# Kernel optimization log

Hardware: AMD Instinct MI355X
Metric: run time of the kernel (lower is better)

## Reference

```python
import jax, jax.numpy as jnp
import numpy as np

B, T, C, NH, L, V = 4, 1024, 768, 12, 4, 512
HD = C // NH
EPS = 1e-5


def setup_inputs() -> dict:
    key = jax.random.key(0)
    ks = jax.random.split(key, 16)
    std = 0.02
    n = lambda k, shape: jax.random.normal(k, shape, jnp.float32) * std
    return {
        "idx": jax.random.randint(ks[0], (B, T), 0, V),
        "tok_emb": n(ks[1], (V, C)),
        "type_emb": n(ks[2], (2, C)),
        "pos_emb": n(ks[3], (1, T, C)),
        "ln1_s": jnp.ones((L, C)), "ln1_b": jnp.zeros((L, C)),
        "ln2_s": jnp.ones((L, C)), "ln2_b": jnp.zeros((L, C)),
        "wq": n(ks[4], (L, C, C)), "bq": jnp.zeros((L, C)),
        "wk": n(ks[5], (L, C, C)), "bk": jnp.zeros((L, C)),
        "wv": n(ks[6], (L, C, C)), "bv": jnp.zeros((L, C)),
        "wp": n(ks[7], (L, C, C)), "bp": jnp.zeros((L, C)),
        "w1": n(ks[8], (L, C, 4 * C)), "b1": jnp.zeros((L, 4 * C)),
        "w2": n(ks[9], (L, 4 * C, C)), "b2": jnp.zeros((L, C)),
        "lnf_s": jnp.ones((C,)), "lnf_b": jnp.zeros((C,)),
        "head_w": n(ks[10], (C, V)),
    }


def _ln(x, s, b):
    m = jnp.mean(x, axis=-1, keepdims=True)
    v = jnp.mean((x - m) ** 2, axis=-1, keepdims=True)
    return (x - m) * jax.lax.rsqrt(v + EPS) * s + b


def _forward(idx, tok_emb, type_emb, pos_emb, ln1_s, ln1_b, ln2_s, ln2_b,
             wq, bq, wk, bk, wv, bv, wp, bp, w1, b1, w2, b2, lnf_s, lnf_b, head_w):
    t = idx.shape[1]
    # token + position + type(=1) embeddings; dropout is identity in eval mode
    x = tok_emb[idx] + pos_emb[:, :t, :] + type_emb[1]
    causal = jnp.tril(jnp.ones((t, t), dtype=bool))  # [T,T]
    scale = 1.0 / np.sqrt(HD)
    attn_maps = []
    for l in range(L):
        h = _ln(x, ln1_s[l], ln1_b[l])
        # project and split heads -> [B,NH,T,HD]
        def heads(w, bb):
            return (h @ w + bb).reshape(B, t, NH, HD).transpose(0, 2, 1, 3)
        q, k, v = heads(wq[l], bq[l]), heads(wk[l], bk[l]), heads(wv[l], bv[l])
        att = jnp.einsum('bhqd,bhkd->bhqk', q, k) * scale
        att = jnp.where(causal, att, -jnp.inf)
        att = jax.nn.softmax(att, axis=-1)
        attn_maps.append(att)
        y = jnp.einsum('bhqk,bhkd->bhqd', att, v)
        y = y.transpose(0, 2, 1, 3).reshape(B, t, C)
        x = x + (y @ wp[l] + bp[l])
        h2 = _ln(x, ln2_s[l], ln2_b[l])
        x = x + (jax.nn.gelu(h2 @ w1[l] + b1[l], approximate=False) @ w2[l] + b2[l])
    x = _ln(x, lnf_s, lnf_b)
    logits = x @ head_w  # head has no bias
    return logits, jnp.stack(attn_maps, axis=0)  # [L,B,NH,T,T]


def reference(idx, tok_emb, type_emb, pos_emb, ln1_s, ln1_b, ln2_s, ln2_b,
              wq, bq, wk, bk, wv, bv, wp, bp, w1, b1, w2, b2, lnf_s, lnf_b, head_w):
    return _forward(idx, tok_emb, type_emb, pos_emb, ln1_s, ln1_b, ln2_s, ln2_b,
                    wq, bq, wk, bk, wv, bv, wp, bp, w1, b1, w2, b2, lnf_s, lnf_b, head_w)
```

## Files before the change

### kernel.cpp

```cpp
#include <hip/hip_runtime.h>
#include <cstdint>


#define B_ 4
#define T_ 1024
#define C_ 768
#define NH_ 12
#define HD_ 64
#define L_ 4
#define V_ 512
#define C4_ 3072

typedef unsigned short u16;
typedef float f32x4 __attribute__((ext_vector_type(4)));
typedef short s16x8 __attribute__((ext_vector_type(8)));
typedef u16 u16x4 __attribute__((ext_vector_type(4)));
typedef u16 u16x8 __attribute__((ext_vector_type(8)));

__device__ __forceinline__ u16 f2b(float f){
  union { float f; unsigned u; } v; v.f = f;
  unsigned u = v.u + 0x7fffu + ((v.u >> 16) & 1u);
  return (u16)(u >> 16);
}

__device__ __forceinline__ unsigned cvtpk(float lo, float hi){
  unsigned r;
  asm("v_cvt_pk_bf16_f32 %0, %1, %2" : "=v"(r) : "v"(lo), "v"(hi));
  return r;
}

__device__ __forceinline__ f32x4 mfma16(s16x8 a, s16x8 b, f32x4 c){
  return __builtin_amdgcn_mfma_f32_16x16x32_bf16(a, b, c, 0, 0, 0);
}

__device__ __forceinline__ void gload16(const void* g, void* l){
  __builtin_amdgcn_global_load_lds((const __attribute__((address_space(1))) unsigned*)g,
                                   (__attribute__((address_space(3))) unsigned*)l, 16, 0, 0);
}

__global__ __launch_bounds__(256) void embed_ln_kernel(const int* __restrict__ idx,
    const float* __restrict__ tok, const float* __restrict__ pos, const float* __restrict__ typ,
    const float* __restrict__ g, const float* __restrict__ bta,
    float* __restrict__ x, u16* __restrict__ out){
  int lane = threadIdx.x & 63;
  int w = threadIdx.x >> 6;
  int row = blockIdx.x*4 + w;
  int t = row & (T_-1);
  int tk = idx[row];
  const float* tr = tok + (size_t)tk*C_;
  const float* pr = pos + (size_t)t*C_;
  float4 v[3];
  float s = 0.f;
  #pragma unroll
  for (int j=0;j<3;j++){
    int c = j*256 + lane*4;
    float4 a = *(const float4*)(tr + c);
    float4 p = *(const float4*)(pr + c);
    float4 ty = *(const float4*)(typ + c);
    v[j] = (float4){a.x+p.x+ty.x, a.y+p.y+ty.y, a.z+p.z+ty.z, a.w+p.w+ty.w};
    s += v[j].x + v[j].y + v[j].z + v[j].w;
  }
  #pragma unroll
  for (int o=32;o>0;o>>=1) s += __shfl_xor(s, o, 64);
  float mean = s * (1.0f/C_);
  float var = 0.f;
  #pragma unroll
  for (int j=0;j<3;j++){
    float dx=v[j].x-mean, dy=v[j].y-mean, dz=v[j].z-mean, dw=v[j].w-mean;
    var += dx*dx+dy*dy+dz*dz+dw*dw;
  }
  #pragma unroll
  for (int o=32;o>0;o>>=1) var += __shfl_xor(var, o, 64);
  float rs = rsqrtf(var*(1.0f/C_) + 1e-5f);
  float* xr = x + (size_t)row*C_;
  u16* orow = out + (size_t)row*C_;
  #pragma unroll
  for (int j=0;j<3;j++){
    int c = j*256 + lane*4;
    *(float4*)(xr + c) = v[j];
    float4 gg = *(const float4*)(g + c);
    float4 bb = *(const float4*)(bta + c);
    u16x4 o = { f2b((v[j].x-mean)*rs*gg.x + bb.x), f2b((v[j].y-mean)*rs*gg.y + bb.y),
                f2b((v[j].z-mean)*rs*gg.z + bb.z), f2b((v[j].w-mean)*rs*gg.w + bb.w) };
    *(u16x4*)(orow + c) = o;
  }
}

__global__ __launch_bounds__(256) void ln_kernel(const float* __restrict__ x,
    const float* __restrict__ g, const float* __restrict__ bta, u16* __restrict__ out){
  int lane = threadIdx.x & 63;
  int row = blockIdx.x*4 + (threadIdx.x >> 6);
  const float* xr = x + (size_t)row*C_;
  float v[12];
  float s = 0.f;
  #pragma unroll
  for (int j=0;j<12;j++){ v[j] = xr[lane + j*64]; s += v[j]; }
  #pragma unroll
  for (int o=32;o>0;o>>=1) s += __shfl_xor(s, o, 64);
  float mean = s * (1.0f/C_);
  float var = 0.f;
  #pragma unroll
  for (int j=0;j<12;j++){ float d = v[j]-mean; var += d*d; }
  #pragma unroll
  for (int o=32;o>0;o>>=1) var += __shfl_xor(var, o, 64);
  float rs = rsqrtf(var*(1.0f/C_) + 1e-5f);
  u16* orow = out + (size_t)row*C_;
  #pragma unroll
  for (int j=0;j<12;j++){ int c = lane+j*64; orow[c] = f2b((v[j]-mean)*rs*g[c] + bta[c]); }
}

struct ConvTable {
  const float* src[7];
  u16* dst[7];
  int K[7], N[7], nTN[7], perZ[7];
  unsigned long long outStride[7];
  int start[8];
};

__global__ __launch_bounds__(256) void convT_all(ConvTable tab){
  int bid = blockIdx.x;
  int d = 0;
  #pragma unroll
  for (int j=1;j<7;j++) if (bid >= tab.start[j]) d = j;
  const float* src = nullptr; u16* dst = nullptr;
  int K=0, N=0, nTN=0, perZ=0; size_t oS=0;
  #pragma unroll
  for (int j=0;j<7;j++) if (d==j){ src=tab.src[j]; dst=tab.dst[j]; K=tab.K[j]; N=tab.N[j];
                                   nTN=tab.nTN[j]; perZ=tab.perZ[j]; oS=(size_t)tab.outStride[j]; }
  int local = bid - tab.start[d];
  int z = local / perZ;
  int rem = local - z*perZ;
  int tk = rem / nTN;
  int tn = rem - tk*nTN;
  int k0 = tk*64, n0 = tn*64;
  size_t inBase = (size_t)z * K * N;
  size_t outBase = (size_t)z * oS;

  __shared__ u16 t[64][68];
  #pragma unroll
  for (int rep=0;rep<4;rep++){
    int id = threadIdx.x + rep*256;
    int kr = id >> 4;
    int nc = (id & 15)*4;
    float4 v = *(const float4*)(src + inBase + (size_t)(k0+kr)*N + n0+nc);
    t[nc+0][kr] = f2b(v.x);
    t[nc+1][kr] = f2b(v.y);
    t[nc+2][kr] = f2b(v.z);
    t[nc+3][kr] = f2b(v.w);
  }
  __syncthreads();
  #pragma unroll
  for (int rep=0;rep<4;rep++){
    int id = threadIdx.x + rep*256;
    int nr = id >> 4;
    int kc = (id & 15)*4;
    u16x4 o = {t[nr][kc], t[nr][kc+1], t[nr][kc+2], t[nr][kc+3]};
    *(u16x4*)(dst + outBase + (size_t)(n0+nr)*K + k0+kc) = o;
  }
}

template<int BM, int MODE, bool GELU>
__global__ __launch_bounds__(256) void gemm_kernel(
    const u16* __restrict__ A, const u16* __restrict__ Bt,
    const float* __restrict__ bias, const float* __restrict__ bias2, const float* __restrict__ bias3,
    u16* __restrict__ outb, u16* __restrict__ outk, u16* __restrict__ outv,
    float* __restrict__ outf, int N, int K)
{
  constexpr int MT = BM/32;
  constexpr int BUF = (BM+128)*64;
  __shared__ u16 smem[2*BUF];
  const int tid = threadIdx.x;
  const int lane = tid & 63;
  const int w = tid >> 6;
  const int wm = w >> 1, wn = w & 1;

  const int gx = gridDim.x;
  const int nwg = gx * gridDim.y;
  int flat = blockIdx.y*gx + blockIdx.x;
  int swzb = (flat & 7)*(nwg >> 3) + (flat >> 3);
  const int m0 = (swzb / gx) * BM;
  const int n0 = (swzb % gx) * 128;

  const int cl = lane & 15, gr = lane >> 4;
  const int rsub = lane >> 3;
  const int swl = ((lane & 7) ^ rsub) * 8;

  f32x4 acc[MT][4];
  #pragma unroll
  for (int a=0;a<MT;a++)
    #pragma unroll
    for (int b=0;b<4;b++) acc[a][b] = (f32x4){0.f,0.f,0.f,0.f};

  auto stage = [&](int kk, u16* buf){
    u16* la = buf;
    u16* lb = buf + BM*64;
    #pragma unroll
    for (int j=0;j<MT;j++){
      int rowb = w*(BM/4) + j*8;
      gload16(A + (size_t)(m0+rowb+rsub)*K + kk + swl, &la[rowb*64]);
    }
    #pragma unroll
    for (int j=0;j<4;j++){
      int rowb = w*32 + j*8;
      gload16(Bt + (size_t)(n0+rowb+rsub)*K + kk + swl, &lb[rowb*64]);
    }
  };

  const int nSteps = K >> 6;
  stage(0, smem);

  for (int t=0; t<nSteps; t++){
    u16* cur = smem + (t&1)*BUF;
    u16* nxt = smem + ((t+1)&1)*BUF;
    if (t+1 < nSteps){
      stage((t+1)<<6, nxt);
      if constexpr (BM==128) asm volatile("s_waitcnt vmcnt(8)" ::: "memory");
      else                   asm volatile("s_waitcnt vmcnt(6)" ::: "memory");
    } else {
      asm volatile("s_waitcnt vmcnt(0)" ::: "memory");
    }
    __builtin_amdgcn_sched_barrier(0);
    __builtin_amdgcn_s_barrier();

    u16* la = cur;
    u16* lb = cur + BM*64;
    #pragma unroll
    for (int cc=0;cc<2;cc++){
      int ko = cc*32 + gr*8;
      s16x8 af[MT], bf[4];
      #pragma unroll
      for (int mt=0;mt<MT;mt++){
        int row = wm*(BM/2) + mt*16 + cl;
        af[mt] = *(const s16x8*)&la[row*64 + (ko ^ ((row&7)*8))];
      }
      #pragma unroll
      for (int nt=0;nt<4;nt++){
        int row = wn*64 + nt*16 + cl;
        bf[nt] = *(const s16x8*)&lb[row*64 + (ko ^ ((row&7)*8))];
      }
      #pragma unroll
      for (int mt=0;mt<MT;mt++)
        #pragma unroll
        for (int nt=0;nt<4;nt++)
          acc[mt][nt] = mfma16(af[mt], bf[nt], acc[mt][nt]);
    }
    __builtin_amdgcn_sched_barrier(0);
    __builtin_amdgcn_s_barrier();
  }

  if (MODE == 5){
    const int which = n0 / C_;
    if (which < 2){
      u16* outp = which ? outk : outb;
      const float* bp = which ? bias2 : bias;
      const int nb = n0 - which*C_;
      #pragma unroll
      for (int mt=0;mt<MT;mt++){
        #pragma unroll
        for (int nt=0;nt<4;nt++){
          #pragma unroll
          for (int i=0;i<4;i++){
            int tl = wm*64 + mt*16 + gr*4 + i;
            int dl = wn*64 + nt*16 + cl;
            smem[tl*128 + (dl ^ ((tl&7)*8))] = f2b(acc[mt][nt][i] + bp[nb + dl]);
          }
        }
      }
      __syncthreads();
      int r = tid >> 1;
      int hloc = tid & 1;
      int h = (nb >> 6) + hloc;
      int b = m0 >> 10, tg = (m0 & (T_-1)) + r;
      u16* orow = outp + (((size_t)b*NH_ + h)*T_ + tg)*HD_;
      #pragma unroll
      for (int j=0;j<8;j++){
        int ch = hloc*8 + j;
        u16x8 vv = *(const u16x8*)&smem[r*128 + ((ch ^ (r&7))*8)];
        *(u16x8*)&orow[j*8] = vv;
      }
    } else {
      const int nb = n0 - 2*C_;
      #pragma unroll
      for (int mt=0;mt<MT;mt++){
        #pragma unroll
        for (int nt=0;nt<4;nt++){
          #pragma unroll
          for (int i=0;i<4;i++){
            int tl = wm*64 + mt*16 + gr*4 + i;
            int dl = wn*64 + nt*16 + cl;
            smem[tl*128 + (dl ^ ((tl&7)*8))] = f2b(acc[mt][nt][i] + bias3[nb + dl]);
          }
        }
      }
      __syncthreads();
      int r = tid & 127, half = tid >> 7;
      int dg = nb + r;
      int h = dg >> 6, dd = dg & (HD_-1);
      int b = m0 >> 10, tg = m0 & (T_-1);
      u16* orow = outv + (((size_t)b*NH_ + h)*HD_ + dd)*T_ + tg;
      #pragma unroll
      for (int j=0;j<8;j++){
        int t0 = half*64 + j*8;
        u16x8 vv;
        #pragma unroll
        for (int s2=0;s2<8;s2++){
          int t = t0 + s2;
          vv[s2] = smem[t*128 + (r ^ ((t&7)*8))];
        }
        *(u16x8*)&orow[t0] = vv;
      }
    }
  } else if (MODE == 0){
    #pragma unroll
    for (int mt=0;mt<MT;mt++){
      #pragma unroll
      for (int nt=0;nt<4;nt++){
        #pragma unroll
        for (int i=0;i<4;i++){
          int tl = wm*64 + mt*16 + gr*4 + i;
          int dl = wn*64 + nt*16 + cl;
          float val = acc[mt][nt][i] + bias[n0 + dl];
          if (GELU) val = 0.5f*val*(1.0f + erff(val*0.70710678118654752440f));
          smem[tl*128 + (dl ^ ((tl&7)*8))] = f2b(val);
        }
      }
    }
    __syncthreads();
    int r = tid >> 1;
    int halfc = tid & 1;
    u16* orow = outb + (size_t)(m0 + r)*N + n0 + halfc*64;
    #pragma unroll
    for (int j=0;j<8;j++){
      int ch = halfc*8 + j;
      u16x8 vv = *(const u16x8*)&smem[r*128 + ((ch ^ (r&7))*8)];
      *(u16x8*)&orow[j*8] = vv;
    }
  } else {
    #pragma unroll
    for (int mt=0;mt<MT;mt++){
      #pragma unroll
      for (int nt=0;nt<4;nt++){
        #pragma unroll
        for (int i=0;i<4;i++){
          int gm = m0 + wm*(BM/2) + mt*16 + gr*4 + i;
          int gn = n0 + wn*64 + nt*16 + cl;
          float val = acc[mt][nt][i];
          if (bias) val += bias[gn];
          if (MODE == 3){
            outf[(size_t)gm*N + gn] += val;
          } else {
            outf[(size_t)gm*N + gn] = val;
          }
        }
      }
    }
  }
}

__global__ __launch_bounds__(256,2) void attn_kernel(
    const u16* __restrict__ q, const u16* __restrict__ k, const u16* __restrict__ vt,
    float* __restrict__ att, u16* __restrict__ y, int layer)
{
  __shared__ u16 pl[4][16*64];
  const int lane = threadIdx.x & 63;
  const int w = threadIdx.x >> 6;
  const int qt = blockIdx.x;
  const int bh = blockIdx.y;
  const int bb = bh / NH_;
  const int hh = bh - bb*NH_;
  const int q0 = qt*64 + w*16;
  const u16* qbase = q + (size_t)bh*T_*HD_;
  const u16* kbase = k + (size_t)bh*T_*HD_;
  const u16* vbase = vt + (size_t)bh*HD_*T_;
  float* abase = att + ((size_t)layer*B_*NH_ + bh)*((size_t)T_*T_);
  u16* plw = &pl[w][0];

  const int cl = lane & 15, gr = lane >> 4;
  const int d0 = gr*8;
  const int swz = (cl & 7)*8;
  const int myq = q0 + cl;

  s16x8 qf0 = *(const s16x8*)(qbase + (size_t)(q0+cl)*HD_ + d0);
  s16x8 qf1 = *(const s16x8*)(qbase + (size_t)(q0+cl)*HD_ + 32 + d0);

  const float scale = 0.125f;
  const int nkt = qt + 1;

  unsigned pbuf[16][8];
  float slocal = 0.f;
  f32x4 yacc[4];
  #pragma unroll
  for (int n=0;n<4;n++) yacc[n] = (f32x4){0.f,0.f,0.f,0.f};

  #pragma unroll
  for (int kt=0; kt<16; kt++){
    if (kt < nkt){
      #pragma unroll
      for (int n=0;n<4;n++){
        int krow = kt*64 + n*16 + cl;
        s16x8 kf0 = *(const s16x8*)(kbase + (size_t)krow*HD_ + d0);
        s16x8 kf1 = *(const s16x8*)(kbase + (size_t)krow*HD_ + 32 + d0);
        f32x4 dacc = (f32x4){0.f,0.f,0.f,0.f};
        dacc = mfma16(kf0, qf0, dacc);
        dacc = mfma16(kf1, qf1, dacc);
        float p[4];
        #pragma unroll
        for (int i=0;i<4;i++){
          float sv = dacc[i]*scale;
          int kk = kt*64 + n*16 + gr*4 + i;
          if (kt == qt && kk > myq) sv = -1e30f;
          p[i] = __expf(sv);
        }
        slocal += (p[0]+p[1]) + (p[2]+p[3]);
        unsigned lo = cvtpk(p[0],p[1]), hi = cvtpk(p[2],p[3]);
        pbuf[kt][2*n]   = lo;
        pbuf[kt][2*n+1] = hi;
        int colb = (n*16 + gr*4) ^ swz;
        *(uint2*)&plw[cl*64 + colb] = make_uint2(lo, hi);
      }
      asm volatile("s_waitcnt lgkmcnt(0)" ::: "memory");
      __builtin_amdgcn_sched_barrier(0);
      #pragma unroll
      for (int cc=0;cc<2;cc++){
        s16x8 pa = *(const s16x8*)&plw[cl*64 + ((cc*32 + d0) ^ swz)];
        #pragma unroll
        for (int n2=0;n2<4;n2++){
          s16x8 bv = *(const s16x8*)(vbase + (size_t)(n2*16+cl)*T_ + kt*64 + cc*32 + d0);
          yacc[n2] = mfma16(pa, bv, yacc[n2]);
        }
      }
    }
  }

  slocal += __shfl_xor(slocal, 16, 64);
  slocal += __shfl_xor(slocal, 32, 64);
  float inv = 1.0f / slocal;

  float invy[4];
  #pragma unroll
  for (int i=0;i<4;i++) invy[i] = __shfl(inv, gr*4 + i, 64);

  #pragma unroll
  for (int n2=0;n2<4;n2++){
    #pragma unroll
    for (int i=0;i<4;i++){
      int r = q0 + gr*4 + i;
      y[((size_t)bb*T_ + r)*C_ + hh*HD_ + n2*16 + cl] = f2b(yacc[n2][i]*invy[i]);
    }
  }

  #pragma unroll
  for (int kt=0; kt<16; kt++){
    if (kt < nkt){
      #pragma unroll
      for (int n=0;n<4;n++){
        unsigned lo = pbuf[kt][2*n], hi = pbuf[kt][2*n+1];
        float p0 = __uint_as_float(lo << 16)          * inv;
        float p1 = __uint_as_float(lo & 0xffff0000u)  * inv;
        float p2 = __uint_as_float(hi << 16)          * inv;
        float p3 = __uint_as_float(hi & 0xffff0000u)  * inv;
        *(float4*)&abase[(size_t)myq*T_ + kt*64 + n*16 + gr*4] = make_float4(p0,p1,p2,p3);
      }
    }
  }

  int kend = nkt*64;
  if (kend < T_){
    int w4 = (T_ - kend) >> 2;
    for (int r = w; r < 64; r += 4){
      float* rp = abase + (size_t)(qt*64 + r)*T_ + kend;
      for (int c = lane; c < w4; c += 64){
        *(float4*)(rp + c*4) = make_float4(0.f,0.f,0.f,0.f);
      }
    }
  }
}

extern "C" void kernel_launch(void* const* d_in, const int* in_sizes, int n_in,
                              void* d_out, int out_size, void* d_ws, size_t ws_size,
                              hipStream_t stream)
{
  (void)in_sizes; (void)n_in; (void)out_size; (void)ws_size;
  const int*   idx  = (const int*)d_in[0];
  const float* tok  = (const float*)d_in[1];
  const float* typ  = (const float*)d_in[2];
  const float* pos  = (const float*)d_in[3];
  const float* ln1s = (const float*)d_in[4];
  const float* ln1b = (const float*)d_in[5];
  const float* ln2s = (const float*)d_in[6];
  const float* ln2b = (const float*)d_in[7];
  const float* wq   = (const float*)d_in[8];
  const float* bq   = (const float*)d_in[9];
  const float* wk   = (const float*)d_in[10];
  const float* bk   = (const float*)d_in[11];
  const float* wv   = (const float*)d_in[12];
  const float* bv   = (const float*)d_in[13];
  const float* wp   = (const float*)d_in[14];
  const float* bp   = (const float*)d_in[15];
  const float* w1   = (const float*)d_in[16];
  const float* b1   = (const float*)d_in[17];
  const float* w2   = (const float*)d_in[18];
  const float* b2   = (const float*)d_in[19];
  const float* lnfs = (const float*)d_in[20];
  const float* lnfb = (const float*)d_in[21];
  const float* hw   = (const float*)d_in[22];

  char* ws = (char*)d_ws;
  float* x    = (float*)(ws + 0);
  u16* hbf    = (u16*)(ws + 12582912);
  u16* qb     = (u16*)(ws + 18874368);
  u16* kb     = (u16*)(ws + 25165824);
  u16* vtb    = (u16*)(ws + 31457280);
  u16* yb     = (u16*)(ws + 37748736);
  u16* h2     = (u16*)(ws + 44040192);
  u16* wqkvT  = (u16*)(ws + 69206016);
  u16* wpT    = (u16*)(ws + 83361792);
  u16* w1T    = (u16*)(ws + 88080384);
  u16* w2T    = (u16*)(ws + 106954752);
  u16* hwT    = (u16*)(ws + 125829120);

  float* logits = (float*)d_out;
  float* att = logits + (size_t)B_*T_*V_;

  const size_t CC   = (size_t)C_*C_;
  const size_t CC4  = (size_t)C_*C4_;
  const size_t QKVL = (size_t)3*C_*C_;

  ConvTable tab;
  const float* srcs[7] = {wq, wk, wv, wp, w1, w2, hw};
  u16* dsts[7] = {wqkvT, wqkvT + CC, wqkvT + 2*CC, wpT, w1T, w2T, hwT};
  int Ks[7]   = {C_, C_, C_, C_, C_,  C4_, C_};
  int Ns[7]   = {C_, C_, C_, C_, C4_, C_,  V_};
  int nzs[7]  = {L_, L_, L_, L_, L_,  L_,  1};
  unsigned long long oss[7] = {QKVL, QKVL, QKVL, CC, CC4, CC4, CC};
  int acc = 0;
  for (int j=0;j<7;j++){
    tab.src[j]=srcs[j]; tab.dst[j]=dsts[j]; tab.K[j]=Ks[j]; tab.N[j]=Ns[j];
    tab.nTN[j]=Ns[j]/64; tab.perZ[j]=(Ks[j]/64)*(Ns[j]/64); tab.outStride[j]=oss[j];
    tab.start[j]=acc; acc += tab.perZ[j]*nzs[j];
  }
  tab.start[7]=acc;
  convT_all<<<acc, 256, 0, stream>>>(tab);

  embed_ln_kernel<<<1024, 256, 0, stream>>>(idx, tok, pos, typ + C_, ln1s, ln1b, x, hbf);

  for (int l=0; l<L_; l++){
    if (l > 0)
      ln_kernel<<<1024, 256, 0, stream>>>(x, ln1s + l*C_, ln1b + l*C_, hbf);
    gemm_kernel<128,5,false><<<dim3(18,32), 256, 0, stream>>>(
        hbf, wqkvT + l*QKVL, bq + l*C_, bk + l*C_, bv + l*C_,
        qb, kb, vtb, nullptr, 3*C_, C_);
    attn_kernel<<<dim3(16,48), 256, 0, stream>>>(qb, kb, vtb, att, yb, l);
    gemm_kernel<128,3,false><<<dim3(6,32), 256, 0, stream>>>(
        yb, wpT + l*CC, bp + l*C_, nullptr, nullptr,
        nullptr, nullptr, nullptr, x, C_, C_);
    ln_kernel<<<1024, 256, 0, stream>>>(x, ln2s + l*C_, ln2b + l*C_, hbf);
    gemm_kernel<128,0,true><<<dim3(24,32), 256, 0, stream>>>(
        hbf, w1T + l*CC4, b1 + l*C4_, nullptr, nullptr,
        h2, nullptr, nullptr, nullptr, C4_, C_);
    gemm_kernel<128,3,false><<<dim3(6,32), 256, 0, stream>>>(
        h2, w2T + l*CC4, b2 + l*C_, nullptr, nullptr,
        nullptr, nullptr, nullptr, x, C_, C4_);
  }
  ln_kernel<<<1024, 256, 0, stream>>>(x, lnfs, lnfb, hbf);
  gemm_kernel<64,4,false><<<dim3(4,64), 256, 0, stream>>>(
      hbf, hwT, nullptr, nullptr, nullptr,
      nullptr, nullptr, nullptr, logits, V_, C_);
}
```

Baseline: 1.237 ms.

## Single-buffer GEMM LDS staging and raise wave priority around attention MFMAs

The GEMM kernel's double-buffered LDS pipeline, which prefetched the next K tile during compute, is replaced by one buffer loaded and then consumed behind __syncthreads each step. This halves LDS use per block and may allow more resident blocks, but global loads no longer overlap with MFMA work. Separately, the attention kernel wraps its MFMA sequences in s_setprio(1)/s_setprio(0) so waves issuing matrix work get scheduling priority.

```diff
diff --git a/kernel.cpp b/kernel.cpp
--- a/kernel.cpp
+++ b/kernel.cpp
@@ -167,8 +167,7 @@
     float* __restrict__ outf, int N, int K)
 {
   constexpr int MT = BM/32;
-  constexpr int BUF = (BM+128)*64;
-  __shared__ u16 smem[2*BUF];
+  __shared__ u16 smem[(BM+128)*64];
   const int tid = threadIdx.x;
   const int lane = tid & 63;
   const int w = tid >> 6;
@@ -191,9 +190,12 @@
     #pragma unroll
     for (int b=0;b<4;b++) acc[a][b] = (f32x4){0.f,0.f,0.f,0.f};
 
-  auto stage = [&](int kk, u16* buf){
-    u16* la = buf;
-    u16* lb = buf + BM*64;
+  u16* la = smem;
+  u16* lb = smem + BM*64;
+
+  const int nSteps = K >> 6;
+  for (int t=0; t<nSteps; t++){
+    const int kk = t << 6;
     #pragma unroll
     for (int j=0;j<MT;j++){
       int rowb = w*(BM/4) + j*8;
@@ -204,26 +206,7 @@
       int rowb = w*32 + j*8;
       gload16(Bt + (size_t)(n0+rowb+rsub)*K + kk + swl, &lb[rowb*64]);
     }
-  };
-
-  const int nSteps = K >> 6;
-  stage(0, smem);
-
-  for (int t=0; t<nSteps; t++){
-    u16* cur = smem + (t&1)*BUF;
-    u16* nxt = smem + ((t+1)&1)*BUF;
-    if (t+1 < nSteps){
-      stage((t+1)<<6, nxt);
-      if constexpr (BM==128) asm volatile("s_waitcnt vmcnt(8)" ::: "memory");
-      else                   asm volatile("s_waitcnt vmcnt(6)" ::: "memory");
-    } else {
-      asm volatile("s_waitcnt vmcnt(0)" ::: "memory");
-    }
-    __builtin_amdgcn_sched_barrier(0);
-    __builtin_amdgcn_s_barrier();
-
-    u16* la = cur;
-    u16* lb = cur + BM*64;
+    __syncthreads();
     #pragma unroll
     for (int cc=0;cc<2;cc++){
       int ko = cc*32 + gr*8;
@@ -244,8 +227,7 @@
         for (int nt=0;nt<4;nt++)
           acc[mt][nt] = mfma16(af[mt], bf[nt], acc[mt][nt]);
     }
-    __builtin_amdgcn_sched_barrier(0);
-    __builtin_amdgcn_s_barrier();
+    __syncthreads();
   }
 
   if (MODE == 5){
@@ -401,8 +383,10 @@
         s16x8 kf0 = *(const s16x8*)(kbase + (size_t)krow*HD_ + d0);
         s16x8 kf1 = *(const s16x8*)(kbase + (size_t)krow*HD_ + 32 + d0);
         f32x4 dacc = (f32x4){0.f,0.f,0.f,0.f};
+        __builtin_amdgcn_s_setprio(1);
         dacc = mfma16(kf0, qf0, dacc);
         dacc = mfma16(kf1, qf1, dacc);
+        __builtin_amdgcn_s_setprio(0);
         float p[4];
         #pragma unroll
         for (int i=0;i<4;i++){
@@ -420,6 +404,7 @@
       }
       asm volatile("s_waitcnt lgkmcnt(0)" ::: "memory");
       __builtin_amdgcn_sched_barrier(0);
+      __builtin_amdgcn_s_setprio(1);
       #pragma unroll
       for (int cc=0;cc<2;cc++){
         s16x8 pa = *(const s16x8*)&plw[cl*64 + ((cc*32 + d0) ^ swz)];
@@ -429,6 +414,7 @@
           yacc[n2] = mfma16(pa, bv, yacc[n2]);
         }
       }
+      __builtin_amdgcn_s_setprio(0);
     }
   }
 
```

After: 1.440 ms. 1.16x slower.

## Switch GEMM to triple-buffered K=32 stages with new LDS swizzle

Applied to the files above, without the earlier changes.

The GEMM mainloop now uses 32-wide K tiles with three LDS buffers and prefetches two stages ahead instead of double-buffering 64-wide tiles. A new XOR swizzle is introduced for the 32-column layout, and the wait counts are adjusted for the tail iterations. The goal is better latency hiding of global loads, at the cost of twice as many barriers per K and smaller MFMA batches between them. A syncthreads is added before the MODE 0 epilogue reuses shared memory.

```diff
diff --git a/kernel.cpp b/kernel.cpp
--- a/kernel.cpp
+++ b/kernel.cpp
@@ -167,8 +167,8 @@
     float* __restrict__ outf, int N, int K)
 {
   constexpr int MT = BM/32;
-  constexpr int BUF = (BM+128)*64;
-  __shared__ u16 smem[2*BUF];
+  constexpr int BUF = (BM+128)*32;
+  __shared__ u16 smem[3*BUF];
   const int tid = threadIdx.x;
   const int lane = tid & 63;
   const int w = tid >> 6;
@@ -182,8 +182,8 @@
   const int n0 = (swzb % gx) * 128;
 
   const int cl = lane & 15, gr = lane >> 4;
-  const int rsub = lane >> 3;
-  const int swl = ((lane & 7) ^ rsub) * 8;
+  const int scol = ((lane & 3) ^ ((lane >> 2) & 3) ^ (lane >> 4)) * 8;
+  const int rslot = (gr ^ (cl & 3) ^ (cl >> 2)) * 8;
 
   f32x4 acc[MT][4];
   #pragma unroll
@@ -191,59 +191,59 @@
     #pragma unroll
     for (int b=0;b<4;b++) acc[a][b] = (f32x4){0.f,0.f,0.f,0.f};
 
-  auto stage = [&](int kk, u16* buf){
+  auto stage = [&](int t, u16* buf){
+    const int kk = t << 5;
     u16* la = buf;
-    u16* lb = buf + BM*64;
-    #pragma unroll
-    for (int j=0;j<MT;j++){
-      int rowb = w*(BM/4) + j*8;
-      gload16(A + (size_t)(m0+rowb+rsub)*K + kk + swl, &la[rowb*64]);
-    }
-    #pragma unroll
-    for (int j=0;j<4;j++){
-      int rowb = w*32 + j*8;
-      gload16(Bt + (size_t)(n0+rowb+rsub)*K + kk + swl, &lb[rowb*64]);
+    u16* lb = buf + BM*32;
+    #pragma unroll
+    for (int jj=0; jj<BM/64; jj++){
+      int row0 = w*(BM/4) + jj*16;
+      gload16(A + (size_t)(m0 + row0 + (lane>>2))*K + kk + scol, &la[row0*32]);
+    }
+    #pragma unroll
+    for (int jj=0; jj<2; jj++){
+      int row0 = w*32 + jj*16;
+      gload16(Bt + (size_t)(n0 + row0 + (lane>>2))*K + kk + scol, &lb[row0*32]);
     }
   };
 
-  const int nSteps = K >> 6;
+  const int nSteps = K >> 5;
   stage(0, smem);
+  stage(1, smem + BUF);
 
   for (int t=0; t<nSteps; t++){
-    u16* cur = smem + (t&1)*BUF;
-    u16* nxt = smem + ((t+1)&1)*BUF;
-    if (t+1 < nSteps){
-      stage((t+1)<<6, nxt);
+    if (t+2 < nSteps){
+      stage(t+2, smem + ((t+2)%3)*BUF);
       if constexpr (BM==128) asm volatile("s_waitcnt vmcnt(8)" ::: "memory");
       else                   asm volatile("s_waitcnt vmcnt(6)" ::: "memory");
+    } else if (t+1 < nSteps){
+      if constexpr (BM==128) asm volatile("s_waitcnt vmcnt(4)" ::: "memory");
+      else                   asm volatile("s_waitcnt vmcnt(3)" ::: "memory");
     } else {
       asm volatile("s_waitcnt vmcnt(0)" ::: "memory");
     }
     __builtin_amdgcn_sched_barrier(0);
     __builtin_amdgcn_s_barrier();
 
-    u16* la = cur;
-    u16* lb = cur + BM*64;
-    #pragma unroll
-    for (int cc=0;cc<2;cc++){
-      int ko = cc*32 + gr*8;
-      s16x8 af[MT], bf[4];
-      #pragma unroll
-      for (int mt=0;mt<MT;mt++){
-        int row = wm*(BM/2) + mt*16 + cl;
-        af[mt] = *(const s16x8*)&la[row*64 + (ko ^ ((row&7)*8))];
-      }
-      #pragma unroll
-      for (int nt=0;nt<4;nt++){
-        int row = wn*64 + nt*16 + cl;
-        bf[nt] = *(const s16x8*)&lb[row*64 + (ko ^ ((row&7)*8))];
-      }
-      #pragma unroll
-      for (int mt=0;mt<MT;mt++)
-        #pragma unroll
-        for (int nt=0;nt<4;nt++)
-          acc[mt][nt] = mfma16(af[mt], bf[nt], acc[mt][nt]);
-    }
+    u16* la = smem + (t%3)*BUF;
+    u16* lb = la + BM*32;
+    s16x8 af[MT], bf[4];
+    #pragma unroll
+    for (int mt=0;mt<MT;mt++){
+      int row = wm*(BM/2) + mt*16 + cl;
+      af[mt] = *(const s16x8*)&la[row*32 + rslot];
+    }
+    #pragma unroll
+    for (int nt=0;nt<4;nt++){
+      int row = wn*64 + nt*16 + cl;
+      bf[nt] = *(const s16x8*)&lb[row*32 + rslot];
+    }
+    #pragma unroll
+    for (int mt=0;mt<MT;mt++)
+      #pragma unroll
+      for (int nt=0;nt<4;nt++)
+        acc[mt][nt] = mfma16(af[mt], bf[nt], acc[mt][nt]);
+
     __builtin_amdgcn_sched_barrier(0);
     __builtin_amdgcn_s_barrier();
   }
@@ -311,6 +311,7 @@
       }
     }
   } else if (MODE == 0){
+    __syncthreads();
     #pragma unroll
     for (int mt=0;mt<MT;mt++){
       #pragma unroll
```

Result: slower. 1.285 ms (+3.9%).
